# Kernel tuning notes

Hardware: AMD Instinct MI355X
Metric: run time of the kernel (lower is better)

The kernel has to match this reference:

```python
import jax, jax.numpy as jnp
import numpy as np

DIM = 64
HEADS = 4
WIN = 4


def setup_inputs() -> dict:
    key = jax.random.key(0)
    ks = jax.random.split(key, 9)
    B, C, D, H, W = 2, DIM, 64, 64, 64
    x = jax.random.normal(ks[0], (B, C, D, H, W), dtype=jnp.float32)
    # 1x1x1 Conv3d == pointwise linear: weight [C_out, C_in], bias [C_out]
    def mk(kw, kb):
        return (jax.random.normal(kw, (C, C), dtype=jnp.float32) * 0.05,
                jax.random.normal(kb, (C,), dtype=jnp.float32) * 0.05)
    Wq, bq = mk(ks[1], ks[2])
    Wk, bk = mk(ks[3], ks[4])
    Wv, bv = mk(ks[5], ks[6])
    Wp, bp = mk(ks[7], ks[8])
    return {"x": x, "Wq": Wq, "bq": bq, "Wk": Wk, "bk": bk,
            "Wv": Wv, "bv": bv, "Wp": Wp, "bp": bp}


def reference(x, Wq, bq, Wk, bk, Wv, bv, Wp, bp):
    B, C, D, H, W = x.shape
    w = WIN
    heads = HEADS
    hd = C // heads
    L = w * w * w  # tokens per window (64)
    nd, nh, nw = D // w, H // w, W // w  # spatial dims are multiples of w -> no padding branch
    scale = hd ** -0.5

    # window partition: [B,C,D,H,W] -> [B*nd*nh*nw, C, L]
    xw = (x.reshape(B, C, nd, w, nh, w, nw, w)
            .transpose(0, 2, 4, 6, 1, 3, 5, 7)
            .reshape(B * nd * nh * nw, C, L))

    def pointwise(t, Wm, bm):  # 1x1x1 conv on flattened windows
        return jnp.einsum('ncl,oc->nol', t, Wm) + bm[None, :, None]

    q = pointwise(xw, Wq, bq).reshape(-1, heads, hd, L)
    k = pointwise(xw, Wk, bk).reshape(-1, heads, hd, L)
    v = pointwise(xw, Wv, bv).reshape(-1, heads, hd, L)

    # attn[n,h,i,j] = <q[:, :, :, i], k[:, :, :, j]> * scale ; softmax over j
    attn = jax.nn.softmax(jnp.einsum('nhdi,nhdj->nhij', q, k) * scale, axis=-1)
    # out = v @ attn^T  (dropout is identity in eval)
    out = jnp.einsum('nhdj,nhij->nhdi', v, attn)

    out = out.reshape(-1, C, L)
    out = pointwise(out, Wp, bp)

    # reverse window partition: [B*nd*nh*nw, C, L] -> [B,C,D,H,W]
    out = (out.reshape(B, nd, nh, nw, C, w, w, w)
              .transpose(0, 4, 1, 5, 2, 6, 3, 7)
              .reshape(B, C, D, H, W))
    return out
```

## Files before the change

### kernel.cpp

```cpp
#include <hip/hip_runtime.h>

typedef _Float16 f16;
typedef __attribute__((ext_vector_type(4))) _Float16 f16x4;
typedef __attribute__((ext_vector_type(8))) _Float16 f16x8;
typedef __attribute__((ext_vector_type(4))) float f32x4;

#define MFMA32(a,b,c) __builtin_amdgcn_mfma_f32_16x16x32_f16((a),(b),(c),0,0,0)
#define MFMA16(a,b,c) __builtin_amdgcn_mfma_f32_16x16x16f16((a),(b),(c),0,0,0)

__global__ void wprep(const float* __restrict__ Wq, const float* __restrict__ Wk,
                      const float* __restrict__ Wv, const float* __restrict__ Wp,
                      f16* __restrict__ ws)
{
    const int t = threadIdx.x;
    const int lane = t & 63;
    const float* Wm[4] = {Wq, Wk, Wv, Wp};
    #pragma unroll
    for (int j = 0; j < 8; ++j) {
        const int c = (t >> 6) * 8 + j;
        const int m = c >> 3, ob = (c >> 1) & 3, s = c & 1;
        const float* src = Wm[m] + (ob * 16 + (lane & 15)) * 64 + 8 * (lane >> 4) + 32 * s;
        f32x4 a4 = *(const f32x4*)src;
        f32x4 b4 = *(const f32x4*)(src + 4);
        f16x8 h;
        #pragma unroll
        for (int ii = 0; ii < 8; ++ii) h[ii] = (f16)(ii < 4 ? a4[ii] : b4[ii - 4]);
        *(f16x8*)(ws + c * 512 + lane * 8) = h;
    }
}

__global__ __launch_bounds__(256, 3)
void wsa3d(const float* __restrict__ x, const f16* __restrict__ wsf,
           const float* __restrict__ bq, const float* __restrict__ bk,
           const float* __restrict__ bv, const float* __restrict__ bp,
           float* __restrict__ out)
{
    __shared__ __align__(16) unsigned char smem[50240];
    f16*   const XW = (f16*)smem;
    float* const SG = (float*)(smem + 32768);

    const int tid  = threadIdx.x;
    const int lane = tid & 63;
    const int w    = tid >> 6;
    const int g    = lane >> 4;
    const int ln16 = lane & 15;
    const int key  = ln16 & 7;

    const int bid = blockIdx.x;
    const int Q   = ((bid & 7) << 8) | (bid >> 3);
    const int qx = Q & 3, ih = (Q >> 2) & 15, idz = (Q >> 6) & 15, b = Q >> 10;

    const float c_sc = 0.25f * 1.44269504088896340736f;
    const f32x4 z4 = {0.f, 0.f, 0.f, 0.f};

    const int gz = (lane >> 4) & 3, gy = (lane >> 2) & 3, gq = lane & 3;

    f32x4 vals[16];
    #pragma unroll
    for (int i = 0; i < 16; ++i) {
        const int c = w * 16 + i;
        vals[i] = *(const f32x4*)(x + ((((b*64 + c)*64 + idz*4 + gz)*64) + ih*4 + gy)*64 + qx*16 + gq*4);
    }
    #pragma unroll
    for (int lx = 0; lx < 4; ++lx) {
        const int t = gz * 16 + gy * 4 + lx;
        #pragma unroll
        for (int h2 = 0; h2 < 2; ++h2) {
            f16x8 pk;
            #pragma unroll
            for (int ii = 0; ii < 8; ++ii) pk[ii] = (f16)vals[h2 * 8 + ii][lx];
            *(f16x8*)(XW + gq*4096 + t*64 + (((w*2 + h2) ^ (t & 7) ^ gq) << 3)) = pk;
        }
    }
    __syncthreads();

    f16x8 xf[4][2];
    #pragma unroll
    for (int lb = 0; lb < 4; ++lb)
        #pragma unroll
        for (int s = 0; s < 2; ++s)
            xf[lb][s] = *(const f16x8*)(XW + w*4096 + (lb*16 + ln16)*64 + (((g + 4*s) ^ key ^ w) << 3));

    #pragma unroll
    for (int ob = 0; ob < 4; ++ob) {
        f16x8 VF[2];
        #pragma unroll
        for (int s = 0; s < 2; ++s) VF[s] = *(const f16x8*)(wsf + (16 + ob*2 + s)*512 + lane*8);
        const float bvo = bv[ob * 16 + ln16];
        #pragma unroll
        for (int tb = 0; tb < 4; ++tb) {
            f32x4 a = z4;
            #pragma unroll
            for (int s = 0; s < 2; ++s) a = MFMA32(xf[tb][s], VF[s], a);
            f16x4 h4;
            #pragma unroll
            for (int r = 0; r < 4; ++r) h4[r] = (f16)(a[r] + bvo);
            *(f16x4*)(XW + w*4096 + (ob*16 + ln16)*64 + (((2*tb + (g >> 1)) ^ key ^ w) << 3) + 4*(g & 1)) = h4;
        }
    }

    f16x4 ot[4][4];
    #pragma unroll
    for (int h = 0; h < 4; ++h) {
        f16x8 QF[2], KF[2];
        #pragma unroll
        for (int s = 0; s < 2; ++s) {
            QF[s] = *(const f16x8*)(wsf + (h*2 + s)*512 + lane*8);
            KF[s] = *(const f16x8*)(wsf + (8 + h*2 + s)*512 + lane*8);
        }
        const f32x4 bqv = *(const f32x4*)(bq + h*16 + g*4);
        const f32x4 bkv = *(const f32x4*)(bk + h*16 + g*4);
        f16x4 qf[4], kf[4];
        #pragma unroll
        for (int lb = 0; lb < 4; ++lb) {
            f32x4 aq = z4, ak = z4;
            #pragma unroll
            for (int s = 0; s < 2; ++s) {
                aq = MFMA32(QF[s], xf[lb][s], aq);
                ak = MFMA32(KF[s], xf[lb][s], ak);
            }
            #pragma unroll
            for (int r = 0; r < 4; ++r) {
                qf[lb][r] = (f16)((aq[r] + bqv[r]) * c_sc);
                kf[lb][r] = (f16)(ak[r] + bkv[r]);
            }
        }
        f16x4 va[4];
        #pragma unroll
        for (int jb = 0; jb < 4; ++jb)
            va[jb] = *(const f16x4*)(XW + w*4096 + (16*h + ln16)*64 + (((2*jb + (g >> 1)) ^ key ^ w) << 3) + 4*(g & 1));
        #pragma unroll
        for (int ib = 0; ib < 4; ++ib) {
            f32x4 e[4];
            #pragma unroll
            for (int jb = 0; jb < 4; ++jb) {
                f32x4 S = MFMA16(kf[jb], qf[ib], z4);
                #pragma unroll
                for (int r = 0; r < 4; ++r) e[jb][r] = __builtin_amdgcn_exp2f(S[r]);
            }
            f32x4 s4 = e[0] + e[1] + e[2] + e[3];
            float hh = (s4[0] + s4[1]) + (s4[2] + s4[3]);
            hh += __shfl_xor(hh, 16);
            hh += __shfl_xor(hh, 32);
            const float inv = __builtin_amdgcn_rcpf(hh);
            f32x4 O = z4;
            #pragma unroll
            for (int jb = 0; jb < 4; ++jb) {
                f16x4 pf;
                #pragma unroll
                for (int r = 0; r < 4; ++r) pf[r] = (f16)e[jb][r];
                O = MFMA16(va[jb], pf, O);
            }
            #pragma unroll
            for (int r = 0; r < 4; ++r) ot[h][ib][r] = (f16)(O[r] * inv);
        }
    }

    #pragma unroll
    for (int h = 0; h < 4; ++h)
        #pragma unroll
        for (int ib = 0; ib < 4; ++ib)
            *(f16x4*)(XW + w*4096 + (16*ib + ln16)*64 + (((2*h + (g >> 1)) ^ key ^ w) << 3) + 4*(g & 1)) = ot[h][ib];

    f16x8 PF[4][2];
    #pragma unroll
    for (int oc = 0; oc < 4; ++oc)
        #pragma unroll
        for (int s = 0; s < 2; ++s) PF[oc][s] = *(const f16x8*)(wsf + (24 + oc*2 + s)*512 + lane*8);
    float bps[4];
    #pragma unroll
    for (int oc = 0; oc < 4; ++oc) bps[oc] = bp[oc * 16 + ln16];

    f32x4 res[4][4];
    #pragma unroll
    for (int tb = 0; tb < 4; ++tb) {
        f16x8 af[2];
        #pragma unroll
        for (int s = 0; s < 2; ++s)
            af[s] = *(const f16x8*)(XW + w*4096 + (tb*16 + ln16)*64 + (((g + 4*s) ^ key ^ w) << 3));
        #pragma unroll
        for (int oc = 0; oc < 4; ++oc) {
            f32x4 a = z4;
            #pragma unroll
            for (int s = 0; s < 2; ++s) a = MFMA32(af[s], PF[oc][s], a);
            #pragma unroll
            for (int r = 0; r < 4; ++r) res[tb][oc][r] = a[r] + bps[oc];
        }
    }

    #pragma unroll
    for (int oc = 0; oc < 4; ++oc) {
        #pragma unroll
        for (int tb = 0; tb < 4; ++tb)
            *(f32x4*)(SG + w*1092 + ln16*68 + ((tb*16 + g*4) ^ (w << 2))) = res[tb][oc];
        __syncthreads();
        #pragma unroll
        for (int si = 0; si < 4; ++si) {
            const int o2 = w * 4 + si;
            f32x4 v4 = *(const f32x4*)(SG + gq*1092 + o2*68 + ((gz*16 + gy*4) ^ (gq << 2)));
            *(f32x4*)(out + ((((b*64 + oc*16 + o2)*64 + idz*4 + gz)*64) + ih*4 + gy)*64 + qx*16 + gq*4) = v4;
        }
        if (oc < 3) __syncthreads();
    }
}

extern "C" void kernel_launch(void* const* d_in, const int* in_sizes, int n_in,
                              void* d_out, int out_size, void* d_ws, size_t ws_size,
                              hipStream_t stream) {
    (void)in_sizes; (void)n_in; (void)out_size; (void)ws_size;
    const float* x  = (const float*)d_in[0];
    const float* Wq = (const float*)d_in[1];
    const float* bq = (const float*)d_in[2];
    const float* Wk = (const float*)d_in[3];
    const float* bk = (const float*)d_in[4];
    const float* Wv = (const float*)d_in[5];
    const float* bv = (const float*)d_in[6];
    const float* Wp = (const float*)d_in[7];
    const float* bp = (const float*)d_in[8];
    f16* wsf = (f16*)d_ws;
    wprep<<<1, 256, 0, stream>>>(Wq, Wk, Wv, Wp, wsf);
    wsa3d<<<2048, 256, 0, stream>>>(x, wsf, bq, bk, bv, bp, (float*)d_out);
}
```

Measured before the change: 68.72 us.

## Alias output staging onto activation LDS to fit four blocks per CU

Shrinks shared memory from about 50KB to 32KB by reusing the activation buffer for the fp32 output staging area, with an extra barrier inserted, and raises the launch-bounds occupancy target from 3 to 4 blocks per CU. Input values are converted to packed fp16 right after loading to cut register pressure. Bias loads are hoisted to the start, and the Q/K weight fragments for the next head are prefetched while the current head is computed. The output projection now computes per output-channel group just before storing, instead of holding all results in registers. The aim is higher occupancy to hide memory latency, at the cost of a tighter register budget that may cause spills.

```diff
diff --git a/kernel.cpp b/kernel.cpp
--- a/kernel.cpp
+++ b/kernel.cpp
@@ -1,12 +1,20 @@
 #include <hip/hip_runtime.h>
 
 typedef _Float16 f16;
+typedef __attribute__((ext_vector_type(2))) _Float16 f16x2;
 typedef __attribute__((ext_vector_type(4))) _Float16 f16x4;
 typedef __attribute__((ext_vector_type(8))) _Float16 f16x8;
+typedef __attribute__((ext_vector_type(2))) __fp16 fp16x2_raw;
 typedef __attribute__((ext_vector_type(4))) float f32x4;
 
 #define MFMA32(a,b,c) __builtin_amdgcn_mfma_f32_16x16x32_f16((a),(b),(c),0,0,0)
 #define MFMA16(a,b,c) __builtin_amdgcn_mfma_f32_16x16x16f16((a),(b),(c),0,0,0)
+
+__device__ __forceinline__ f16x2 cvt2(float a, float b) {
+    fp16x2_raw v = __builtin_amdgcn_cvt_pkrtz(a, b);
+    f16x2 r; __builtin_memcpy(&r, &v, sizeof(r));
+    return r;
+}
 
 __global__ void wprep(const float* __restrict__ Wq, const float* __restrict__ Wk,
                       const float* __restrict__ Wv, const float* __restrict__ Wp,
@@ -29,15 +37,15 @@
     }
 }
 
-__global__ __launch_bounds__(256, 3)
+__global__ __launch_bounds__(256, 4)
 void wsa3d(const float* __restrict__ x, const f16* __restrict__ wsf,
            const float* __restrict__ bq, const float* __restrict__ bk,
            const float* __restrict__ bv, const float* __restrict__ bp,
            float* __restrict__ out)
 {
-    __shared__ __align__(16) unsigned char smem[50240];
-    f16*   const XW = (f16*)smem;
-    float* const SG = (float*)(smem + 32768);
+    __shared__ __align__(16) f16 lds[16384];
+    f16*   const XW = lds;
+    float* const SG = (float*)lds;
 
     const int tid  = threadIdx.x;
     const int lane = tid & 63;
@@ -55,12 +63,24 @@
 
     const int gz = (lane >> 4) & 3, gy = (lane >> 2) & 3, gq = lane & 3;
 
-    f32x4 vals[16];
+    f16x4 valh[16];
     #pragma unroll
     for (int i = 0; i < 16; ++i) {
         const int c = w * 16 + i;
-        vals[i] = *(const f32x4*)(x + ((((b*64 + c)*64 + idz*4 + gz)*64) + ih*4 + gy)*64 + qx*16 + gq*4);
-    }
+        f32x4 v4 = *(const f32x4*)(x + ((((b*64 + c)*64 + idz*4 + gz)*64) + ih*4 + gy)*64 + qx*16 + gq*4);
+        f16x2 lo = cvt2(v4[0], v4[1]), hi = cvt2(v4[2], v4[3]);
+        valh[i] = f16x4{lo[0], lo[1], hi[0], hi[1]};
+    }
+    f32x4 bqv[4], bkv[4];
+    float bvs4[4], bps4[4];
+    #pragma unroll
+    for (int h = 0; h < 4; ++h) {
+        bqv[h] = *(const f32x4*)(bq + h * 16 + g * 4);
+        bkv[h] = *(const f32x4*)(bk + h * 16 + g * 4);
+        bvs4[h] = bv[h * 16 + ln16];
+        bps4[h] = bp[h * 16 + ln16];
+    }
+
     #pragma unroll
     for (int lx = 0; lx < 4; ++lx) {
         const int t = gz * 16 + gy * 4 + lx;
@@ -68,7 +88,7 @@
         for (int h2 = 0; h2 < 2; ++h2) {
             f16x8 pk;
             #pragma unroll
-            for (int ii = 0; ii < 8; ++ii) pk[ii] = (f16)vals[h2 * 8 + ii][lx];
+            for (int ii = 0; ii < 8; ++ii) pk[ii] = valh[h2 * 8 + ii][lx];
             *(f16x8*)(XW + gq*4096 + t*64 + (((w*2 + h2) ^ (t & 7) ^ gq) << 3)) = pk;
         }
     }
@@ -81,12 +101,18 @@
         for (int s = 0; s < 2; ++s)
             xf[lb][s] = *(const f16x8*)(XW + w*4096 + (lb*16 + ln16)*64 + (((g + 4*s) ^ key ^ w) << 3));
 
+    f16x8 QF[2], KF[2];
+    #pragma unroll
+    for (int s = 0; s < 2; ++s) {
+        QF[s] = *(const f16x8*)(wsf + (0*2 + s)*512 + lane*8);
+        KF[s] = *(const f16x8*)(wsf + (8 + 0*2 + s)*512 + lane*8);
+    }
+
     #pragma unroll
     for (int ob = 0; ob < 4; ++ob) {
         f16x8 VF[2];
         #pragma unroll
         for (int s = 0; s < 2; ++s) VF[s] = *(const f16x8*)(wsf + (16 + ob*2 + s)*512 + lane*8);
-        const float bvo = bv[ob * 16 + ln16];
         #pragma unroll
         for (int tb = 0; tb < 4; ++tb) {
             f32x4 a = z4;
@@ -94,7 +120,7 @@
             for (int s = 0; s < 2; ++s) a = MFMA32(xf[tb][s], VF[s], a);
             f16x4 h4;
             #pragma unroll
-            for (int r = 0; r < 4; ++r) h4[r] = (f16)(a[r] + bvo);
+            for (int r = 0; r < 4; ++r) h4[r] = (f16)(a[r] + bvs4[ob]);
             *(f16x4*)(XW + w*4096 + (ob*16 + ln16)*64 + (((2*tb + (g >> 1)) ^ key ^ w) << 3) + 4*(g & 1)) = h4;
         }
     }
@@ -102,14 +128,6 @@
     f16x4 ot[4][4];
     #pragma unroll
     for (int h = 0; h < 4; ++h) {
-        f16x8 QF[2], KF[2];
-        #pragma unroll
-        for (int s = 0; s < 2; ++s) {
-            QF[s] = *(const f16x8*)(wsf + (h*2 + s)*512 + lane*8);
-            KF[s] = *(const f16x8*)(wsf + (8 + h*2 + s)*512 + lane*8);
-        }
-        const f32x4 bqv = *(const f32x4*)(bq + h*16 + g*4);
-        const f32x4 bkv = *(const f32x4*)(bk + h*16 + g*4);
         f16x4 qf[4], kf[4];
         #pragma unroll
         for (int lb = 0; lb < 4; ++lb) {
@@ -121,8 +139,15 @@
             }
             #pragma unroll
             for (int r = 0; r < 4; ++r) {
-                qf[lb][r] = (f16)((aq[r] + bqv[r]) * c_sc);
-                kf[lb][r] = (f16)(ak[r] + bkv[r]);
+                qf[lb][r] = (f16)((aq[r] + bqv[h][r]) * c_sc);
+                kf[lb][r] = (f16)(ak[r] + bkv[h][r]);
+            }
+        }
+        if (h < 3) {
+            #pragma unroll
+            for (int s = 0; s < 2; ++s) {
+                QF[s] = *(const f16x8*)(wsf + ((h+1)*2 + s)*512 + lane*8);
+                KF[s] = *(const f16x8*)(wsf + (8 + (h+1)*2 + s)*512 + lane*8);
             }
         }
         f16x4 va[4];
@@ -162,37 +187,30 @@
         for (int ib = 0; ib < 4; ++ib)
             *(f16x4*)(XW + w*4096 + (16*ib + ln16)*64 + (((2*h + (g >> 1)) ^ key ^ w) << 3) + 4*(g & 1)) = ot[h][ib];
 
+    f16x8 af[4][2];
+    #pragma unroll
+    for (int tb = 0; tb < 4; ++tb)
+        #pragma unroll
+        for (int s = 0; s < 2; ++s)
+            af[tb][s] = *(const f16x8*)(XW + w*4096 + (tb*16 + ln16)*64 + (((g + 4*s) ^ key ^ w) << 3));
     f16x8 PF[4][2];
     #pragma unroll
     for (int oc = 0; oc < 4; ++oc)
         #pragma unroll
         for (int s = 0; s < 2; ++s) PF[oc][s] = *(const f16x8*)(wsf + (24 + oc*2 + s)*512 + lane*8);
-    float bps[4];
-    #pragma unroll
-    for (int oc = 0; oc < 4; ++oc) bps[oc] = bp[oc * 16 + ln16];
-
-    f32x4 res[4][4];
-    #pragma unroll
-    for (int tb = 0; tb < 4; ++tb) {
-        f16x8 af[2];
-        #pragma unroll
-        for (int s = 0; s < 2; ++s)
-            af[s] = *(const f16x8*)(XW + w*4096 + (tb*16 + ln16)*64 + (((g + 4*s) ^ key ^ w) << 3));
-        #pragma unroll
-        for (int oc = 0; oc < 4; ++oc) {
+    __syncthreads();
+
+    #pragma unroll
+    for (int oc = 0; oc < 4; ++oc) {
+        #pragma unroll
+        for (int tb = 0; tb < 4; ++tb) {
             f32x4 a = z4;
             #pragma unroll
-            for (int s = 0; s < 2; ++s) a = MFMA32(af[s], PF[oc][s], a);
-            #pragma unroll
-            for (int r = 0; r < 4; ++r) res[tb][oc][r] = a[r] + bps[oc];
-        }
-    }
-
-    #pragma unroll
-    for (int oc = 0; oc < 4; ++oc) {
-        #pragma unroll
-        for (int tb = 0; tb < 4; ++tb)
-            *(f32x4*)(SG + w*1092 + ln16*68 + ((tb*16 + g*4) ^ (w << 2))) = res[tb][oc];
+            for (int s = 0; s < 2; ++s) a = MFMA32(af[tb][s], PF[oc][s], a);
+            #pragma unroll
+            for (int r = 0; r < 4; ++r) a[r] += bps4[oc];
+            *(f32x4*)(SG + w*1092 + ln16*68 + ((tb*16 + g*4) ^ (w << 2))) = a;
+        }
         __syncthreads();
         #pragma unroll
         for (int si = 0; si < 4; ++si) {
```

Measured after the change: 119.4 us. 1.74x slower.
